# Performance work log

Measured on AMD Instinct MI355X. Metric: run time of the kernel, lower is better.

Reference implementation:

```python
import jax, jax.numpy as jnp
import numpy as np

T, B, D, O, U = 64, 32768, 6, 3, 6


def setup_inputs() -> dict:
    key = jax.random.key(0)
    ks = jax.random.split(key, 8)
    measurements = jax.random.normal(ks[0], (T, B, O), dtype=jnp.float32)
    inputs_seq = jax.random.normal(ks[1], (T, B, U), dtype=jnp.float32)
    mean0 = jax.random.normal(ks[2], (B, D), dtype=jnp.float32)
    # initial covariance: 0.1 * I, positive definite
    cov0 = jnp.broadcast_to(0.1 * jnp.eye(D, dtype=jnp.float32), (B, D, D))
    # linear motion model params (jacobian = A), kept near-stable
    A = jnp.eye(D, dtype=jnp.float32) + 0.01 * jax.random.normal(ks[3], (D, D), dtype=jnp.float32)
    Bm = 0.1 * jax.random.normal(ks[4], (D, U), dtype=jnp.float32)
    Q_tril = jnp.tril(0.05 * jax.random.normal(ks[5], (D, D), dtype=jnp.float32)) + 0.1 * jnp.eye(D, dtype=jnp.float32)
    # linear measurement model params (jacobian = C)
    C = jax.random.normal(ks[6], (O, D), dtype=jnp.float32) / np.sqrt(D)
    R_tril = jnp.tril(0.05 * jax.random.normal(ks[7], (O, O), dtype=jnp.float32)) + 0.1 * jnp.eye(O, dtype=jnp.float32)
    return {"measurements": measurements, "inputs_seq": inputs_seq, "mean0": mean0,
            "cov0": cov0, "A": A, "Bm": Bm, "Q_tril": Q_tril, "C": C, "R_tril": R_tril}


def reference(measurements, inputs_seq, mean0, cov0, A, Bm, Q_tril, C, R_tril):
    Qc = Q_tril @ Q_tril.T            # (D, D) dynamics covariance
    Rc = R_tril @ R_tril.T            # (O, O) measurement covariance
    I = jnp.eye(mean0.shape[-1], dtype=mean0.dtype)

    def step(carry, xs):
        mean, cov = carry             # (B, D), (B, D, D)
        z, u = xs                     # (B, O), (B, U)
        # --- predict ---
        pred_mean = mean @ A.T + u @ Bm.T                        # (B, D)
        pred_cov = jnp.einsum('ij,bjk,lk->bil', A, cov, A) + Qc  # (B, D, D)
        # --- update ---
        pred_meas = pred_mean @ C.T                              # (B, O)
        innovation = z - pred_meas
        S = jnp.einsum('ij,bjk,lk->bil', C, pred_cov, C) + Rc    # (B, O, O)
        PCt = jnp.einsum('bij,kj->bik', pred_cov, C)             # (B, D, O)
        K = PCt @ jnp.linalg.inv(S)                              # (B, D, O)
        new_mean = pred_mean + jnp.einsum('bij,bj->bi', K, innovation)
        new_cov = (I - jnp.einsum('bij,jk->bik', K, C)) @ pred_cov
        return (new_mean, new_cov), new_mean

    (_, _), means = jax.lax.scan(step, (mean0, cov0), (measurements, inputs_seq))
    return means  # (T, B, D)
```

## Files before the change

### kernel.cpp

```cpp
#include <hip/hip_runtime.h>


#define T_STEPS 64
#define BATCH   32768
#define NCOEF   90
#define NCHUNK  8
#define CLEN    8

#define G_OFF   23040
#define GV_OFF  24192
#define WS_NEED (GV_OFF + NCHUNK * BATCH * 6 * 4)

__device__ __forceinline__ float rdlane(float v, int lane) {
    return __int_as_float(__builtin_amdgcn_readlane(__float_as_int(v), lane));
}

__global__ __launch_bounds__(64) void ekf_precompute(
    const float* __restrict__ cov0, const float* __restrict__ Ag,
    const float* __restrict__ Bg,   const float* __restrict__ Qtg,
    const float* __restrict__ Cg,   const float* __restrict__ Rtg,
    float* __restrict__ coef, float* __restrict__ Gmat, int writeG)
{
    __shared__ float sA[36], sB[36], sC[18], sQt[36], sRt[9];
    __shared__ float Qc[36], Rc[9];
    __shared__ float Mall[T_STEPS * 36];
    const int tid = threadIdx.x;

    if (tid < 36) { sA[tid] = Ag[tid]; sB[tid] = Bg[tid]; sQt[tid] = Qtg[tid]; }
    if (tid < 18) sC[tid] = Cg[tid];
    if (tid < 9)  sRt[tid] = Rtg[tid];
    __syncthreads();

    if (tid < 36) {
        int i = tid / 6, j = tid % 6; float s = 0.f;
        #pragma unroll
        for (int k = 0; k < 6; ++k) s += sQt[i*6+k] * sQt[j*6+k];
        Qc[tid] = s;
    } else if (tid < 45) {
        int q = tid - 36, i = q / 3, j = q % 3; float s = 0.f;
        #pragma unroll
        for (int k = 0; k < 3; ++k) s += sRt[i*3+k] * sRt[j*3+k];
        Rc[q] = s;
    }
    __syncthreads();

    const int i6 = tid / 6, j6 = tid % 6;
    const int i3 = tid / 3, j3 = tid % 3;
    const int qS = (tid >= 36 && tid < 45) ? tid - 36 : 0;
    const int sa = qS / 3, sb = qS % 3;

    float Ai[6], Aj[6], Acol[6], Bcol[6], Cst[18], Crow[6], Ca[6];
    float qcv = 0.f, rcv = 0.f;
    #pragma unroll
    for (int l = 0; l < 6; ++l) { Ai[l]=0.f; Aj[l]=0.f; Acol[l]=0.f; Bcol[l]=0.f; Crow[l]=0.f; Ca[l]=0.f; }
    #pragma unroll
    for (int l = 0; l < 18; ++l) Cst[l] = 0.f;

    if (tid < 36) {
        #pragma unroll
        for (int l = 0; l < 6; ++l) {
            Ai[l] = sA[i6*6+l]; Aj[l] = sA[j6*6+l];
            Acol[l] = sA[l*6+j6]; Bcol[l] = sB[l*6+j6];
        }
        #pragma unroll
        for (int l = 0; l < 18; ++l) Cst[l] = sC[l];
        qcv = Qc[tid];
    }
    if (tid < 18) {
        #pragma unroll
        for (int l = 0; l < 6; ++l) Crow[l] = sC[j3*6+l];
    }
    if (tid >= 36 && tid < 45) {
        #pragma unroll
        for (int l = 0; l < 6; ++l) Ca[l] = sC[sa*6+l];
        rcv = Rc[qS];
    }

    float Preg = 0.f;
    if (tid < 36) Preg = cov0[tid];
    __syncthreads();

    for (int t = 0; t < T_STEPS; ++t) {
        float Pf[36];
        #pragma unroll
        for (int e = 0; e < 36; ++e) Pf[e] = rdlane(Preg, e);
        float p1 = qcv;
        #pragma unroll
        for (int k = 0; k < 6; ++k) {
            float tmp = 0.f;
            #pragma unroll
            for (int l = 0; l < 6; ++l) tmp += Pf[k*6+l] * Aj[l];
            p1 += Ai[k] * tmp;
        }

        float p1r[6];
        #pragma unroll
        for (int l = 0; l < 6; ++l) p1r[l] = __shfl(p1, i3*6 + l);
        float pct = p1r[0]*Crow[0] + p1r[1]*Crow[1] + p1r[2]*Crow[2]
                  + p1r[3]*Crow[3] + p1r[4]*Crow[4] + p1r[5]*Crow[5];

        float sv = rcv;
        #pragma unroll
        for (int l = 0; l < 6; ++l) sv += Ca[l] * __shfl(pct, l*3 + sb);

        float a  = rdlane(sv, 36), b  = rdlane(sv, 37), c  = rdlane(sv, 38);
        float d  = rdlane(sv, 39), e  = rdlane(sv, 40), f  = rdlane(sv, 41);
        float g  = rdlane(sv, 42), h  = rdlane(sv, 43), i9 = rdlane(sv, 44);
        float idet = 1.0f / (a*(e*i9-f*h) - b*(d*i9-f*g) + c*(d*h-e*g));
        float s0 =  (e*i9-f*h)*idet, s1 = -(b*i9-c*h)*idet, s2 =  (b*f-c*e)*idet;
        float s3 = -(d*i9-f*g)*idet, s4 =  (a*i9-c*g)*idet, s5 = -(a*f-c*d)*idet;
        float s6 =  (d*h-e*g)*idet,  s7 = -(a*h-b*g)*idet,  s8 =  (a*e-b*d)*idet;

        float Pi0 = __shfl(pct, i6*3 + 0);
        float Pi1 = __shfl(pct, i6*3 + 1);
        float Pi2 = __shfl(pct, i6*3 + 2);
        float K0 = Pi0*s0 + Pi1*s3 + Pi2*s6;
        float K1 = Pi0*s1 + Pi1*s4 + Pi2*s7;
        float K2 = Pi0*s2 + Pi1*s5 + Pi2*s8;

        float ik[6];
        #pragma unroll
        for (int k = 0; k < 6; ++k)
            ik[k] = ((i6 == k) ? 1.f : 0.f)
                  - (K0*Cst[0*6+k] + K1*Cst[1*6+k] + K2*Cst[2*6+k]);

        float p1col[6];
        #pragma unroll
        for (int k = 0; k < 6; ++k) p1col[k] = __shfl(p1, k*6 + j6);

        float mo = 0.f, no = 0.f, pn = 0.f;
        #pragma unroll
        for (int k = 0; k < 6; ++k) {
            mo += ik[k] * Acol[k];
            no += ik[k] * Bcol[k];
            pn += ik[k] * p1col[k];
        }

        if (tid < 36) {
            coef[t*NCOEF + tid]      = mo;
            coef[t*NCOEF + 36 + tid] = no;
            if (j6 < 3)
                coef[t*NCOEF + 72 + i6*3 + j6] = (j6 == 0 ? K0 : (j6 == 1 ? K1 : K2));
            Mall[t*36 + tid] = mo;
        }
        Preg = pn;
    }
    __syncthreads();

    if (writeG) {
        const int im = (tid < 36) ? i6 : 0;
        for (int cch = 0; cch < NCHUNK; ++cch) {
            float Gv = (tid < 36) ? Mall[(cch*CLEN)*36 + tid] : 0.f;
            for (int s = 1; s < CLEN; ++s) {
                float acc = 0.f;
                #pragma unroll
                for (int k = 0; k < 6; ++k) {
                    float gk = __shfl(Gv, k*6 + j6);
                    acc += Mall[(cch*CLEN + s)*36 + im*6 + k] * gk;
                }
                Gv = acc;
            }
            if (tid < 36) Gmat[cch*36 + tid] = Gv;
        }
    }
}

__global__ __launch_bounds__(256) void ekf_gpass(
    const float* __restrict__ z, const float* __restrict__ u,
    const float* __restrict__ coef, float* __restrict__ g)
{
    const int c = blockIdx.y;
    const int b = blockIdx.x * 256 + threadIdx.x;

    float m[6] = {0.f, 0.f, 0.f, 0.f, 0.f, 0.f};

    #pragma unroll
    for (int s = 0; s < CLEN; ++s) {
        const int t = c * CLEN + s;
        const float* cf = coef + t * NCOEF;
        const int base  = t * BATCH + b;

        const float*  zp = z + (size_t)base * 3;
        const float2* up = (const float2*)(u + (size_t)base * 6);
        float zz[3] = { zp[0], zp[1], zp[2] };
        float2 u01 = up[0], u23 = up[1], u45 = up[2];
        float uu[6] = { u01.x, u01.y, u23.x, u23.y, u45.x, u45.y };

        float nm[6];
        #pragma unroll
        for (int i = 0; i < 6; ++i) {
            float s2 = 0.f;
            #pragma unroll
            for (int j = 0; j < 6; ++j) s2 += cf[i*6+j] * m[j];
            #pragma unroll
            for (int j = 0; j < 6; ++j) s2 += cf[36 + i*6 + j] * uu[j];
            #pragma unroll
            for (int j = 0; j < 3; ++j) s2 += cf[72 + i*3 + j] * zz[j];
            nm[i] = s2;
        }
        #pragma unroll
        for (int i = 0; i < 6; ++i) m[i] = nm[i];
    }

    float2* gp = (float2*)(g + ((size_t)c * BATCH + b) * 6);
    gp[0] = make_float2(m[0], m[1]);
    gp[1] = make_float2(m[2], m[3]);
    gp[2] = make_float2(m[4], m[5]);
}

__global__ __launch_bounds__(256) void ekf_opass(
    const float* __restrict__ z, const float* __restrict__ u,
    const float* __restrict__ mean0, const float* __restrict__ coef,
    const float* __restrict__ Gmat, const float* __restrict__ g,
    float* __restrict__ out)
{
    const int c = blockIdx.y;
    const int b = blockIdx.x * 256 + threadIdx.x;

    float m[6];
    {
        const float2* mp = (const float2*)(mean0 + (size_t)b * 6);
        float2 a0 = mp[0], a1 = mp[1], a2 = mp[2];
        m[0]=a0.x; m[1]=a0.y; m[2]=a1.x; m[3]=a1.y; m[4]=a2.x; m[5]=a2.y;
    }

    for (int cc = 0; cc < c; ++cc) {
        const float* G = Gmat + cc * 36;
        const float2* gp = (const float2*)(g + ((size_t)cc * BATCH + b) * 6);
        float2 g01 = gp[0], g23 = gp[1], g45 = gp[2];
        float gv[6] = { g01.x, g01.y, g23.x, g23.y, g45.x, g45.y };
        float nm[6];
        #pragma unroll
        for (int i = 0; i < 6; ++i) {
            float s2 = gv[i];
            #pragma unroll
            for (int j = 0; j < 6; ++j) s2 += G[i*6+j] * m[j];
            nm[i] = s2;
        }
        #pragma unroll
        for (int i = 0; i < 6; ++i) m[i] = nm[i];
    }

    #pragma unroll
    for (int s = 0; s < CLEN; ++s) {
        const int t = c * CLEN + s;
        const float* cf = coef + t * NCOEF;
        const int base  = t * BATCH + b;

        const float*  zp = z + (size_t)base * 3;
        const float2* up = (const float2*)(u + (size_t)base * 6);
        float zz[3] = { zp[0], zp[1], zp[2] };
        float2 u01 = up[0], u23 = up[1], u45 = up[2];
        float uu[6] = { u01.x, u01.y, u23.x, u23.y, u45.x, u45.y };

        float nm[6];
        #pragma unroll
        for (int i = 0; i < 6; ++i) {
            float s2 = 0.f;
            #pragma unroll
            for (int j = 0; j < 6; ++j) s2 += cf[i*6+j] * m[j];
            #pragma unroll
            for (int j = 0; j < 6; ++j) s2 += cf[36 + i*6 + j] * uu[j];
            #pragma unroll
            for (int j = 0; j < 3; ++j) s2 += cf[72 + i*3 + j] * zz[j];
            nm[i] = s2;
        }

        float2* op = (float2*)(out + (size_t)base * 6);
        op[0] = make_float2(nm[0], nm[1]);
        op[1] = make_float2(nm[2], nm[3]);
        op[2] = make_float2(nm[4], nm[5]);

        #pragma unroll
        for (int i = 0; i < 6; ++i) m[i] = nm[i];
    }
}

__global__ __launch_bounds__(128) void ekf_mean(
    const float* __restrict__ z, const float* __restrict__ u,
    const float* __restrict__ mean0, const float* __restrict__ coef,
    float* __restrict__ out)
{
    __shared__ float sc[T_STEPS * NCOEF];
    const int tid = threadIdx.x;
    for (int idx = tid; idx < T_STEPS * NCOEF; idx += 128) sc[idx] = coef[idx];

    const int b = blockIdx.x * 128 + tid;
    float m[6];
    {
        const float2* mp = (const float2*)(mean0 + b * 6);
        float2 a0 = mp[0], a1 = mp[1], a2 = mp[2];
        m[0]=a0.x; m[1]=a0.y; m[2]=a1.x; m[3]=a1.y; m[4]=a2.x; m[5]=a2.y;
    }
    __syncthreads();

    #pragma unroll 2
    for (int t = 0; t < T_STEPS; ++t) {
        const float* cf  = &sc[t * NCOEF];
        const int base   = t * BATCH + b;
        const float*  zp = z + base * 3;
        const float2* up = (const float2*)(u + (size_t)base * 6);

        float zz[3] = { zp[0], zp[1], zp[2] };
        float2 u01 = up[0], u23 = up[1], u45 = up[2];
        float uu[6] = { u01.x, u01.y, u23.x, u23.y, u45.x, u45.y };

        float nm[6];
        #pragma unroll
        for (int i = 0; i < 6; ++i) {
            float s = 0.f;
            #pragma unroll
            for (int j = 0; j < 6; ++j) s += cf[i*6+j] * m[j];
            #pragma unroll
            for (int j = 0; j < 6; ++j) s += cf[36 + i*6 + j] * uu[j];
            #pragma unroll
            for (int j = 0; j < 3; ++j) s += cf[72 + i*3 + j] * zz[j];
            nm[i] = s;
        }

        float2* op = (float2*)(out + (size_t)base * 6);
        op[0] = make_float2(nm[0], nm[1]);
        op[1] = make_float2(nm[2], nm[3]);
        op[2] = make_float2(nm[4], nm[5]);

        #pragma unroll
        for (int i = 0; i < 6; ++i) m[i] = nm[i];
    }
}

extern "C" void kernel_launch(void* const* d_in, const int* in_sizes, int n_in,
                              void* d_out, int out_size, void* d_ws, size_t ws_size,
                              hipStream_t stream) {
    const float* meas  = (const float*)d_in[0];
    const float* useq  = (const float*)d_in[1];
    const float* mean0 = (const float*)d_in[2];
    const float* cov0  = (const float*)d_in[3];
    const float* A     = (const float*)d_in[4];
    const float* Bm    = (const float*)d_in[5];
    const float* Qt    = (const float*)d_in[6];
    const float* C     = (const float*)d_in[7];
    const float* Rt    = (const float*)d_in[8];
    float* out  = (float*)d_out;

    float* coef = (float*)d_ws;
    float* Gmat = (float*)((char*)d_ws + G_OFF);
    float* gvec = (float*)((char*)d_ws + GV_OFF);

    const bool scan_path = (ws_size >= (size_t)WS_NEED);

    ekf_precompute<<<1, 64, 0, stream>>>(cov0, A, Bm, Qt, C, Rt, coef, Gmat,
                                         scan_path ? 1 : 0);
    if (scan_path) {
        dim3 grid(BATCH / 256, NCHUNK);
        ekf_gpass<<<grid, 256, 0, stream>>>(meas, useq, coef, gvec);
        ekf_opass<<<grid, 256, 0, stream>>>(meas, useq, mean0, coef, Gmat, gvec, out);
    } else {
        ekf_mean<<<BATCH / 128, 128, 0, stream>>>(meas, useq, mean0, coef, out);
    }
}
```

Before: 191.4 us.

## Fuse covariance precompute into gpass with flag-based producer/consumer overlap

Result: slower. 253.4 us (+32.4%).

```diff
diff --git a/kernel.cpp b/kernel.cpp
--- a/kernel.cpp
+++ b/kernel.cpp
@@ -9,10 +9,314 @@
 
 #define G_OFF   23040
 #define GV_OFF  24192
-#define WS_NEED (GV_OFF + NCHUNK * BATCH * 6 * 4)
+#define FL_OFF  (GV_OFF + NCHUNK * BATCH * 6 * 4)
+#define WS_NEED (FL_OFF + 4)
 
 __device__ __forceinline__ float rdlane(float v, int lane) {
     return __int_as_float(__builtin_amdgcn_readlane(__float_as_int(v), lane));
+}
+
+__device__ __forceinline__ void wave_lds_sync() {
+    asm volatile("s_waitcnt lgkmcnt(0)" ::: "memory");
+    __builtin_amdgcn_wave_barrier();
+}
+
+__global__ __launch_bounds__(256, 4) void ekf_fused(
+    const float* __restrict__ z, const float* __restrict__ u,
+    const float* __restrict__ cov0, const float* __restrict__ Ag,
+    const float* __restrict__ Bg,   const float* __restrict__ Qtg,
+    const float* __restrict__ Cg,   const float* __restrict__ Rtg,
+    float* __restrict__ coef, float* __restrict__ Gmat,
+    float* __restrict__ g, unsigned int* __restrict__ flag)
+{
+    __shared__ float sA[36], sB[36], sC[18], sQt[36], sRt[9];
+    __shared__ float Qc[36], Rc[9];
+    __shared__ float Mall[T_STEPS * 36];
+    __shared__ float scoef[CLEN * NCOEF];
+
+    const int tid = threadIdx.x;
+    const int c   = blockIdx.y;
+    const int b   = blockIdx.x * 256 + tid;
+    const bool prodWave = (blockIdx.x == 0 && blockIdx.y == 0 && tid < 64);
+
+    if (prodWave) {
+        if (tid < 36) { sA[tid] = Ag[tid]; sB[tid] = Bg[tid]; sQt[tid] = Qtg[tid]; }
+        if (tid < 18) sC[tid] = Cg[tid];
+        if (tid < 9)  sRt[tid] = Rtg[tid];
+        wave_lds_sync();
+
+        if (tid < 36) {
+            int i = tid / 6, j = tid % 6; float s = 0.f;
+            #pragma unroll
+            for (int k = 0; k < 6; ++k) s += sQt[i*6+k] * sQt[j*6+k];
+            Qc[tid] = s;
+        } else if (tid < 45) {
+            int q = tid - 36, i = q / 3, j = q % 3; float s = 0.f;
+            #pragma unroll
+            for (int k = 0; k < 3; ++k) s += sRt[i*3+k] * sRt[j*3+k];
+            Rc[q] = s;
+        }
+        wave_lds_sync();
+
+        const int i6 = tid / 6, j6 = tid % 6;
+        const int i3 = tid / 3, j3 = tid % 3;
+        const int qS = (tid >= 36 && tid < 45) ? tid - 36 : 0;
+        const int sa = qS / 3, sb = qS % 3;
+
+        float Ai[6], Aj[6], Acol[6], Bcol[6], Cst[18], Crow[6], Ca[6];
+        float qcv = 0.f, rcv = 0.f;
+        #pragma unroll
+        for (int l = 0; l < 6; ++l) { Ai[l]=0.f; Aj[l]=0.f; Acol[l]=0.f; Bcol[l]=0.f; Crow[l]=0.f; Ca[l]=0.f; }
+        #pragma unroll
+        for (int l = 0; l < 18; ++l) Cst[l] = 0.f;
+
+        if (tid < 36) {
+            #pragma unroll
+            for (int l = 0; l < 6; ++l) {
+                Ai[l] = sA[i6*6+l]; Aj[l] = sA[j6*6+l];
+                Acol[l] = sA[l*6+j6]; Bcol[l] = sB[l*6+j6];
+            }
+            #pragma unroll
+            for (int l = 0; l < 18; ++l) Cst[l] = sC[l];
+            qcv = Qc[tid];
+        }
+        if (tid < 18) {
+            #pragma unroll
+            for (int l = 0; l < 6; ++l) Crow[l] = sC[j3*6+l];
+        }
+        if (tid >= 36 && tid < 45) {
+            #pragma unroll
+            for (int l = 0; l < 6; ++l) Ca[l] = sC[sa*6+l];
+            rcv = Rc[qS];
+        }
+
+        float Preg = 0.f;
+        if (tid < 36) Preg = cov0[tid];
+        wave_lds_sync();
+
+        for (int t = 0; t < T_STEPS; ++t) {
+            float Pf[36];
+            #pragma unroll
+            for (int e = 0; e < 36; ++e) Pf[e] = rdlane(Preg, e);
+            float p1 = qcv;
+            #pragma unroll
+            for (int k = 0; k < 6; ++k) {
+                float tmp = 0.f;
+                #pragma unroll
+                for (int l = 0; l < 6; ++l) tmp += Pf[k*6+l] * Aj[l];
+                p1 += Ai[k] * tmp;
+            }
+
+            float p1r[6];
+            #pragma unroll
+            for (int l = 0; l < 6; ++l) p1r[l] = __shfl(p1, i3*6 + l);
+            float pct = p1r[0]*Crow[0] + p1r[1]*Crow[1] + p1r[2]*Crow[2]
+                      + p1r[3]*Crow[3] + p1r[4]*Crow[4] + p1r[5]*Crow[5];
+
+            float sv = rcv;
+            #pragma unroll
+            for (int l = 0; l < 6; ++l) sv += Ca[l] * __shfl(pct, l*3 + sb);
+
+            float a  = rdlane(sv, 36), bq = rdlane(sv, 37), cq = rdlane(sv, 38);
+            float d  = rdlane(sv, 39), e  = rdlane(sv, 40), f  = rdlane(sv, 41);
+            float gq = rdlane(sv, 42), h  = rdlane(sv, 43), i9 = rdlane(sv, 44);
+            float idet = 1.0f / (a*(e*i9-f*h) - bq*(d*i9-f*gq) + cq*(d*h-e*gq));
+            float s0 =  (e*i9-f*h)*idet, s1 = -(bq*i9-cq*h)*idet, s2 =  (bq*f-cq*e)*idet;
+            float s3 = -(d*i9-f*gq)*idet, s4 =  (a*i9-cq*gq)*idet, s5 = -(a*f-cq*d)*idet;
+            float s6 =  (d*h-e*gq)*idet,  s7 = -(a*h-bq*gq)*idet,  s8 =  (a*e-bq*d)*idet;
+
+            float Pi0 = __shfl(pct, i6*3 + 0);
+            float Pi1 = __shfl(pct, i6*3 + 1);
+            float Pi2 = __shfl(pct, i6*3 + 2);
+            float K0 = Pi0*s0 + Pi1*s3 + Pi2*s6;
+            float K1 = Pi0*s1 + Pi1*s4 + Pi2*s7;
+            float K2 = Pi0*s2 + Pi1*s5 + Pi2*s8;
+
+            float ik[6];
+            #pragma unroll
+            for (int k = 0; k < 6; ++k)
+                ik[k] = ((i6 == k) ? 1.f : 0.f)
+                      - (K0*Cst[0*6+k] + K1*Cst[1*6+k] + K2*Cst[2*6+k]);
+
+            float p1col[6];
+            #pragma unroll
+            for (int k = 0; k < 6; ++k) p1col[k] = __shfl(p1, k*6 + j6);
+
+            float mo = 0.f, no = 0.f, pn = 0.f;
+            #pragma unroll
+            for (int k = 0; k < 6; ++k) {
+                mo += ik[k] * Acol[k];
+                no += ik[k] * Bcol[k];
+                pn += ik[k] * p1col[k];
+            }
+
+            if (tid < 36) {
+                coef[t*NCOEF + tid]      = mo;
+                coef[t*NCOEF + 36 + tid] = no;
+                if (j6 < 3)
+                    coef[t*NCOEF + 72 + i6*3 + j6] = (j6 == 0 ? K0 : (j6 == 1 ? K1 : K2));
+                Mall[t*36 + tid] = mo;
+            }
+            Preg = pn;
+        }
+
+        __threadfence();
+        if (tid == 0)
+            __hip_atomic_store(flag, 1u, __ATOMIC_RELEASE, __HIP_MEMORY_SCOPE_AGENT);
+
+        wave_lds_sync();
+        {
+            const int im = (tid < 36) ? i6 : 0;
+            for (int cch = 0; cch < NCHUNK; ++cch) {
+                float Gv = (tid < 36) ? Mall[(cch*CLEN)*36 + tid] : 0.f;
+                for (int s = 1; s < CLEN; ++s) {
+                    float acc = 0.f;
+                    #pragma unroll
+                    for (int k = 0; k < 6; ++k) {
+                        float gk = __shfl(Gv, k*6 + j6);
+                        acc += Mall[(cch*CLEN + s)*36 + im*6 + k] * gk;
+                    }
+                    Gv = acc;
+                }
+                if (tid < 36) Gmat[cch*36 + tid] = Gv;
+            }
+        }
+    } else {
+        float acc = 0.f;
+        #pragma unroll
+        for (int s = 0; s < CLEN; ++s) {
+            const int base = (c * CLEN + s) * BATCH + b;
+            const float*  zp = z + (size_t)base * 3;
+            const float2* up = (const float2*)(u + (size_t)base * 6);
+            acc += zp[0] + zp[1] + zp[2];
+            float2 a0 = up[0], a1 = up[1], a2 = up[2];
+            acc += a0.x + a0.y + a1.x + a1.y + a2.x + a2.y;
+        }
+        asm volatile("" :: "v"(acc));
+
+        if (blockIdx.x != 0 || blockIdx.y != 0) {
+            if (tid == 0) {
+                while (__hip_atomic_load(flag, __ATOMIC_RELAXED,
+                                         __HIP_MEMORY_SCOPE_AGENT) == 0u)
+                    __builtin_amdgcn_s_sleep(32);
+            }
+        }
+    }
+
+    __syncthreads();
+    __threadfence();
+
+    {
+        const float* src = coef + c * CLEN * NCOEF;
+        for (int idx = tid; idx < CLEN * NCOEF; idx += 256)
+            scoef[idx] = __hip_atomic_load(src + idx, __ATOMIC_RELAXED,
+                                           __HIP_MEMORY_SCOPE_AGENT);
+    }
+    __syncthreads();
+
+    {
+        float m[6] = {0.f, 0.f, 0.f, 0.f, 0.f, 0.f};
+
+        #pragma unroll
+        for (int s = 0; s < CLEN; ++s) {
+            const float* cf = &scoef[s * NCOEF];
+            const int base  = (c * CLEN + s) * BATCH + b;
+
+            const float*  zp = z + (size_t)base * 3;
+            const float2* up = (const float2*)(u + (size_t)base * 6);
+            float zz[3] = { zp[0], zp[1], zp[2] };
+            float2 u01 = up[0], u23 = up[1], u45 = up[2];
+            float uu[6] = { u01.x, u01.y, u23.x, u23.y, u45.x, u45.y };
+
+            float nm[6];
+            #pragma unroll
+            for (int i = 0; i < 6; ++i) {
+                float s2 = 0.f;
+                #pragma unroll
+                for (int j = 0; j < 6; ++j) s2 += cf[i*6+j] * m[j];
+                #pragma unroll
+                for (int j = 0; j < 6; ++j) s2 += cf[36 + i*6 + j] * uu[j];
+                #pragma unroll
+                for (int j = 0; j < 3; ++j) s2 += cf[72 + i*3 + j] * zz[j];
+                nm[i] = s2;
+            }
+            #pragma unroll
+            for (int i = 0; i < 6; ++i) m[i] = nm[i];
+        }
+
+        float2* gp = (float2*)(g + ((size_t)c * BATCH + b) * 6);
+        gp[0] = make_float2(m[0], m[1]);
+        gp[1] = make_float2(m[2], m[3]);
+        gp[2] = make_float2(m[4], m[5]);
+    }
+}
+
+__global__ __launch_bounds__(256) void ekf_opass(
+    const float* __restrict__ z, const float* __restrict__ u,
+    const float* __restrict__ mean0, const float* __restrict__ coef,
+    const float* __restrict__ Gmat, const float* __restrict__ g,
+    float* __restrict__ out)
+{
+    const int c = blockIdx.y;
+    const int b = blockIdx.x * 256 + threadIdx.x;
+
+    float m[6];
+    {
+        const float2* mp = (const float2*)(mean0 + (size_t)b * 6);
+        float2 a0 = mp[0], a1 = mp[1], a2 = mp[2];
+        m[0]=a0.x; m[1]=a0.y; m[2]=a1.x; m[3]=a1.y; m[4]=a2.x; m[5]=a2.y;
+    }
+
+    for (int cc = 0; cc < c; ++cc) {
+        const float* G = Gmat + cc * 36;
+        const float2* gp = (const float2*)(g + ((size_t)cc * BATCH + b) * 6);
+        float2 g01 = gp[0], g23 = gp[1], g45 = gp[2];
+        float gv[6] = { g01.x, g01.y, g23.x, g23.y, g45.x, g45.y };
+        float nm[6];
+        #pragma unroll
+        for (int i = 0; i < 6; ++i) {
+            float s2 = gv[i];
+            #pragma unroll
+            for (int j = 0; j < 6; ++j) s2 += G[i*6+j] * m[j];
+            nm[i] = s2;
+        }
+        #pragma unroll
+        for (int i = 0; i < 6; ++i) m[i] = nm[i];
+    }
+
+    #pragma unroll
+    for (int s = 0; s < CLEN; ++s) {
+        const int t = c * CLEN + s;
+        const float* cf = coef + t * NCOEF;
+        const int base  = t * BATCH + b;
+
+        const float*  zp = z + (size_t)base * 3;
+        const float2* up = (const float2*)(u + (size_t)base * 6);
+        float zz[3] = { zp[0], zp[1], zp[2] };
+        float2 u01 = up[0], u23 = up[1], u45 = up[2];
+        float uu[6] = { u01.x, u01.y, u23.x, u23.y, u45.x, u45.y };
+
+        float nm[6];
+        #pragma unroll
+        for (int i = 0; i < 6; ++i) {
+            float s2 = 0.f;
+            #pragma unroll
+            for (int j = 0; j < 6; ++j) s2 += cf[i*6+j] * m[j];
+            #pragma unroll
+            for (int j = 0; j < 6; ++j) s2 += cf[36 + i*6 + j] * uu[j];
+            #pragma unroll
+            for (int j = 0; j < 3; ++j) s2 += cf[72 + i*3 + j] * zz[j];
+            nm[i] = s2;
+        }
+
+        float2* op = (float2*)(out + (size_t)base * 6);
+        op[0] = make_float2(nm[0], nm[1]);
+        op[1] = make_float2(nm[2], nm[3]);
+        op[2] = make_float2(nm[4], nm[5]);
+
+        #pragma unroll
+        for (int i = 0; i < 6; ++i) m[i] = nm[i];
+    }
 }
 
 __global__ __launch_bounds__(64) void ekf_precompute(
@@ -162,117 +466,6 @@
             }
             if (tid < 36) Gmat[cch*36 + tid] = Gv;
         }
-    }
-}
-
-__global__ __launch_bounds__(256) void ekf_gpass(
-    const float* __restrict__ z, const float* __restrict__ u,
-    const float* __restrict__ coef, float* __restrict__ g)
-{
-    const int c = blockIdx.y;
-    const int b = blockIdx.x * 256 + threadIdx.x;
-
-    float m[6] = {0.f, 0.f, 0.f, 0.f, 0.f, 0.f};
-
-    #pragma unroll
-    for (int s = 0; s < CLEN; ++s) {
-        const int t = c * CLEN + s;
-        const float* cf = coef + t * NCOEF;
-        const int base  = t * BATCH + b;
-
-        const float*  zp = z + (size_t)base * 3;
-        const float2* up = (const float2*)(u + (size_t)base * 6);
-        float zz[3] = { zp[0], zp[1], zp[2] };
-        float2 u01 = up[0], u23 = up[1], u45 = up[2];
-        float uu[6] = { u01.x, u01.y, u23.x, u23.y, u45.x, u45.y };
-
-        float nm[6];
-        #pragma unroll
-        for (int i = 0; i < 6; ++i) {
-            float s2 = 0.f;
-            #pragma unroll
-            for (int j = 0; j < 6; ++j) s2 += cf[i*6+j] * m[j];
-            #pragma unroll
-            for (int j = 0; j < 6; ++j) s2 += cf[36 + i*6 + j] * uu[j];
-            #pragma unroll
-            for (int j = 0; j < 3; ++j) s2 += cf[72 + i*3 + j] * zz[j];
-            nm[i] = s2;
-        }
-        #pragma unroll
-        for (int i = 0; i < 6; ++i) m[i] = nm[i];
-    }
-
-    float2* gp = (float2*)(g + ((size_t)c * BATCH + b) * 6);
-    gp[0] = make_float2(m[0], m[1]);
-    gp[1] = make_float2(m[2], m[3]);
-    gp[2] = make_float2(m[4], m[5]);
-}
-
-__global__ __launch_bounds__(256) void ekf_opass(
-    const float* __restrict__ z, const float* __restrict__ u,
-    const float* __restrict__ mean0, const float* __restrict__ coef,
-    const float* __restrict__ Gmat, const float* __restrict__ g,
-    float* __restrict__ out)
-{
-    const int c = blockIdx.y;
-    const int b = blockIdx.x * 256 + threadIdx.x;
-
-    float m[6];
-    {
-        const float2* mp = (const float2*)(mean0 + (size_t)b * 6);
-        float2 a0 = mp[0], a1 = mp[1], a2 = mp[2];
-        m[0]=a0.x; m[1]=a0.y; m[2]=a1.x; m[3]=a1.y; m[4]=a2.x; m[5]=a2.y;
-    }
-
-    for (int cc = 0; cc < c; ++cc) {
-        const float* G = Gmat + cc * 36;
-        const float2* gp = (const float2*)(g + ((size_t)cc * BATCH + b) * 6);
-        float2 g01 = gp[0], g23 = gp[1], g45 = gp[2];
-        float gv[6] = { g01.x, g01.y, g23.x, g23.y, g45.x, g45.y };
-        float nm[6];
-        #pragma unroll
-        for (int i = 0; i < 6; ++i) {
-            float s2 = gv[i];
-            #pragma unroll
-            for (int j = 0; j < 6; ++j) s2 += G[i*6+j] * m[j];
-            nm[i] = s2;
-        }
-        #pragma unroll
-        for (int i = 0; i < 6; ++i) m[i] = nm[i];
-    }
-
-    #pragma unroll
-    for (int s = 0; s < CLEN; ++s) {
-        const int t = c * CLEN + s;
-        const float* cf = coef + t * NCOEF;
-        const int base  = t * BATCH + b;
-
-        const float*  zp = z + (size_t)base * 3;
-        const float2* up = (const float2*)(u + (size_t)base * 6);
-        float zz[3] = { zp[0], zp[1], zp[2] };
-        float2 u01 = up[0], u23 = up[1], u45 = up[2];
-        float uu[6] = { u01.x, u01.y, u23.x, u23.y, u45.x, u45.y };
-
-        float nm[6];
-        #pragma unroll
-        for (int i = 0; i < 6; ++i) {
-            float s2 = 0.f;
-            #pragma unroll
-            for (int j = 0; j < 6; ++j) s2 += cf[i*6+j] * m[j];
-            #pragma unroll
-            for (int j = 0; j < 6; ++j) s2 += cf[36 + i*6 + j] * uu[j];
-            #pragma unroll
-            for (int j = 0; j < 3; ++j) s2 += cf[72 + i*3 + j] * zz[j];
-            nm[i] = s2;
-        }
-
-        float2* op = (float2*)(out + (size_t)base * 6);
-        op[0] = make_float2(nm[0], nm[1]);
-        op[1] = make_float2(nm[2], nm[3]);
-        op[2] = make_float2(nm[4], nm[5]);
-
-        #pragma unroll
-        for (int i = 0; i < 6; ++i) m[i] = nm[i];
     }
 }
 
@@ -345,16 +538,18 @@
     float* coef = (float*)d_ws;
     float* Gmat = (float*)((char*)d_ws + G_OFF);
     float* gvec = (float*)((char*)d_ws + GV_OFF);
+    unsigned int* flag = (unsigned int*)((char*)d_ws + FL_OFF);
 
     const bool scan_path = (ws_size >= (size_t)WS_NEED);
 
-    ekf_precompute<<<1, 64, 0, stream>>>(cov0, A, Bm, Qt, C, Rt, coef, Gmat,
-                                         scan_path ? 1 : 0);
     if (scan_path) {
+        hipMemsetAsync(flag, 0, sizeof(unsigned int), stream);
         dim3 grid(BATCH / 256, NCHUNK);
-        ekf_gpass<<<grid, 256, 0, stream>>>(meas, useq, coef, gvec);
+        ekf_fused<<<grid, 256, 0, stream>>>(meas, useq, cov0, A, Bm, Qt, C, Rt,
+                                            coef, Gmat, gvec, flag);
         ekf_opass<<<grid, 256, 0, stream>>>(meas, useq, mean0, coef, Gmat, gvec, out);
     } else {
+        ekf_precompute<<<1, 64, 0, stream>>>(cov0, A, Bm, Qt, C, Rt, coef, Gmat, 0);
         ekf_mean<<<BATCH / 128, 128, 0, stream>>>(meas, useq, mean0, coef, out);
     }
 }
```
